# Performance work log

Hardware: AMD Instinct MI355X
Metric: run time of the kernel (lower is better)

The kernel has to match this reference:

```python
import jax, jax.numpy as jnp
import numpy as np

B, S, D, I, L, H, F = 4, 512, 768, 64, 2, 12, 3072
DH = D // H
LN_EPS = 1e-12


def setup_inputs() -> dict:
    key = jax.random.key(0)
    ks = jax.random.split(key, 24)
    nrm = lambda k, sh, s=0.02: jax.random.normal(k, sh, jnp.float32) * s
    return {
        'hs0': nrm(ks[0], (B, S, D), 1.0),
        'hs1': nrm(ks[1], (B, S, D), 1.0),
        'hs2': nrm(ks[2], (B, S, D), 1.0),
        'Wq': nrm(ks[3], (L, D, D)), 'bq': jnp.zeros((L, D), jnp.float32),
        'Wk': nrm(ks[4], (L, D, D)), 'bk': jnp.zeros((L, D), jnp.float32),
        'Wv': nrm(ks[5], (L, D, D)), 'bv': jnp.zeros((L, D), jnp.float32),
        'Wo': nrm(ks[6], (L, D, D)), 'bo': jnp.zeros((L, D), jnp.float32),
        'ln1_g': jnp.ones((L, D), jnp.float32), 'ln1_b': jnp.zeros((L, D), jnp.float32),
        'W1': nrm(ks[7], (L, D, F)), 'b1': jnp.zeros((L, F), jnp.float32),
        'W2': nrm(ks[8], (L, F, D)), 'b2': jnp.zeros((L, D), jnp.float32),
        'ln2_g': jnp.ones((L, D), jnp.float32), 'ln2_b': jnp.zeros((L, D), jnp.float32),
        'zero_context': nrm(ks[9], (D,), 1.0),
        'ck2tok_mask': jax.random.uniform(ks[10], (B, I, S)) > 0.7,  # True = token excluded from span
        'span_size_ids': jax.random.randint(ks[11], (B, I), 0, 10),
    }


def _ln(x, g, b):
    m = jnp.mean(x, axis=-1, keepdims=True)
    v = jnp.mean((x - m) ** 2, axis=-1, keepdims=True)
    return (x - m) * jax.lax.rsqrt(v + LN_EPS) * g + b


def _forward(hs0, hs1, Wq, bq, Wk, bk, Wv, bv, Wo, bo, ln1_g, ln1_b,
             W1, b1, W2, b2, ln2_g, ln2_b, zero_context, mask):
    # mask: [B,I,S] bool, True = excluded token
    zero_indic = jnp.all(mask, axis=-1)                 # [B,I] spans with no valid token
    mask = mask & ~zero_indic[:, :, None]               # unmask degenerate rows (replaced at end)
    # masked max pooling (init aggregation) -- [B,I,S,D] intermediate, traffic-bound
    pooled = jnp.max(jnp.where(mask[..., None], -jnp.inf, hs0[:, None, :, :]), axis=2)  # [B,I,D]
    ext = (mask.astype(jnp.float32) * -10000.0)[:, None, :, :]  # [B,1,I,S] extended attn mask
    q = pooled
    hs_list = (hs0, hs1)
    inv_sqrt_dh = np.float32(1.0 / np.sqrt(DH))
    for i in range(L):
        hs = hs_list[i]
        qh = (q @ Wq[i] + bq[i]).reshape(B, I, H, DH).transpose(0, 2, 1, 3)   # [B,H,I,DH]
        kh = (hs @ Wk[i] + bk[i]).reshape(B, S, H, DH).transpose(0, 2, 1, 3)  # [B,H,S,DH]
        vh = (hs @ Wv[i] + bv[i]).reshape(B, S, H, DH).transpose(0, 2, 1, 3)
        scores = jnp.einsum('bhid,bhsd->bhis', qh, kh) * inv_sqrt_dh + ext
        attn = jax.nn.softmax(scores, axis=-1)
        ctx = jnp.einsum('bhis,bhsd->bhid', attn, vh).transpose(0, 2, 1, 3).reshape(B, I, D)
        q = _ln(q + ctx @ Wo[i] + bo[i], ln1_g[i], ln1_b[i])
        ffn = jax.nn.gelu(q @ W1[i] + b1[i], approximate=False) @ W2[i] + b2[i]
        q = _ln(q + ffn, ln2_g[i], ln2_b[i])
    # zero-context substitution for empty spans
    return jnp.where(zero_indic[..., None], zero_context, q)


def reference(hs0, hs1, hs2, Wq, bq, Wk, bk, Wv, bv, Wo, bo, ln1_g, ln1_b,
              W1, b1, W2, b2, ln2_g, ln2_b, zero_context, ck2tok_mask, span_size_ids):
    # hs2 is the last entry of the (num_layers+1) slice; query layers 0..L-1 attend hs0..hs1.
    # span_size_ids unused since use_init_size_emb=False.
    del hs2, span_size_ids
    return _forward(hs0, hs1, Wq, bq, Wk, bk, Wv, bv, Wo, bo, ln1_g, ln1_b,
                    W1, b1, W2, b2, ln2_g, ln2_b, zero_context, ck2tok_mask)
```

## Files before the change

kernel.cpp:

```cpp
#include <hip/hip_runtime.h>
#include <hip/hip_bf16.h>
#include <math.h>

#define BB 4
#define SS 512
#define DD 768
#define II 64
#define LL 2
#define HH 12
#define FF 3072

using short8 = __attribute__((ext_vector_type(8))) short;
using f32x4  = __attribute__((ext_vector_type(4))) float;

__device__ __forceinline__ unsigned short f2bf(float x) {
  return __builtin_bit_cast(unsigned short, __float2bfloat16(x));
}

__device__ __forceinline__ void gload_lds16(const void* g, void* l) {
  __builtin_amdgcn_global_load_lds((const __attribute__((address_space(1))) unsigned int*)g,
                                   (__attribute__((address_space(3))) unsigned int*)l, 16, 0, 0);
}

__global__ __launch_bounds__(256) void castmask_kernel(
    const float* __restrict__ hs0, const float* __restrict__ hs1,
    unsigned short* __restrict__ hsb0, unsigned short* __restrict__ hsb1,
    const int* __restrict__ mask, int* __restrict__ zi,
    unsigned long long* __restrict__ pmask, unsigned char* __restrict__ emask) {
  int id = blockIdx.x, t = threadIdx.x;
  if (id < 1536) {
    int idx = id * 256 + t;
    float4 va = ((const float4*)hs0)[idx];
    float4 vb = ((const float4*)hs1)[idx];
    union { unsigned short u[4]; uint2 v; } pa, pb;
    pa.u[0] = f2bf(va.x); pa.u[1] = f2bf(va.y); pa.u[2] = f2bf(va.z); pa.u[3] = f2bf(va.w);
    pb.u[0] = f2bf(vb.x); pb.u[1] = f2bf(vb.y); pb.u[2] = f2bf(vb.z); pb.u[3] = f2bf(vb.w);
    ((uint2*)hsb0)[idx] = pa.v;
    ((uint2*)hsb1)[idx] = pb.v;
  } else {
    int bi = id - 1536;
    int w = t >> 6;
    const int* mrow = mask + (size_t)bi * SS;
    int m0v = mrow[t], m1v = mrow[t + 256];
    int incl = (m0v == 0) | (m1v == 0);
    int any = __syncthreads_or(incl);
    int z = !any;
    unsigned long long w0 = __ballot(z || (m0v == 0));
    unsigned long long w1 = __ballot(z || (m1v == 0));
    if ((t & 63) == 0) {
      pmask[bi * 8 + w] = w0;
      pmask[bi * 8 + 4 + w] = w1;
      if (t == 0) zi[bi] = z;
    }
    emask[(size_t)bi * SS + t] = (unsigned char)((!z) & (m0v != 0));
    emask[(size_t)bi * SS + t + 256] = (unsigned char)((!z) & (m1v != 0));
  }
}

struct TC { const float* s[6]; };

__global__ __launch_bounds__(256) void tcast_kernel(TC src, unsigned short* __restrict__ WT4,
                                                    unsigned short* __restrict__ W1T,
                                                    unsigned short* __restrict__ W2T) {
  __shared__ float smem[8192];
  int id = blockIdx.x, t = threadIdx.x;
  const float* Ws; unsigned short* WTs; int K, N, k0, n0;
  if (id < 576) {
    int z = id / 72, rem = id - z * 72;
    int widx = z >> 1, l = z & 1;
    Ws = src.s[widx] + (size_t)l * DD * DD;
    WTs = WT4 + ((size_t)widx * 2 + l) * DD * DD;
    K = DD; N = DD; k0 = (rem / 6) * 64; n0 = (rem % 6) * 128;
  } else if (id < 1152) {
    int j = id - 576, l = j / 288, rem = j - l * 288;
    Ws = src.s[4] + (size_t)l * DD * FF;
    WTs = W1T + (size_t)l * FF * DD;
    K = DD; N = FF; k0 = (rem / 24) * 64; n0 = (rem % 24) * 128;
  } else {
    int j = id - 1152, l = j / 288, rem = j - l * 288;
    Ws = src.s[5] + (size_t)l * FF * DD;
    WTs = W2T + (size_t)l * DD * FF;
    K = FF; N = DD; k0 = (rem / 6) * 64; n0 = (rem % 6) * 128;
  }
  int w = t >> 6, lane = t & 63;
  #pragma unroll
  for (int cc = 0; cc < 8; ++cc) {
    int c = w * 8 + cc;
    int row = c * 2 + (lane >> 5);
    int cbyte = (lane & 31) * 16;
    int scb = cbyte ^ ((row & 7) << 4);
    gload_lds16((const char*)(Ws + (size_t)(k0 + row) * N + n0) + scb, (char*)smem + c * 1024);
  }
  __syncthreads();
  int n = t >> 1, kh = t & 1;
  union { unsigned short u[32]; uint4 v4[4]; } pk;
  #pragma unroll
  for (int i = 0; i < 32; ++i) {
    int kl = kh * 32 + i;
    float f = *(const float*)((const char*)smem + kl * 512 + ((n * 4) ^ ((kl & 7) << 4)));
    pk.u[i] = f2bf(f);
  }
  uint4* dst = (uint4*)(WTs + (size_t)(n0 + n) * K + k0 + kh * 32);
  dst[0] = pk.v4[0]; dst[1] = pk.v4[1]; dst[2] = pk.v4[2]; dst[3] = pk.v4[3];
}

__global__ __launch_bounds__(256) void pool3_kernel(const float* __restrict__ hs0,
                                                    const unsigned char* __restrict__ emask,
                                                    float* __restrict__ qf,
                                                    unsigned short* __restrict__ qb) {
  __shared__ float eadd[SS];
  int bi = blockIdx.x, dz = blockIdx.y;
  int b = bi >> 6, t = threadIdx.x;
  if (t < 128) {
    uchar4 e4 = ((const uchar4*)(emask + (size_t)bi * SS))[t];
    const float NEG = -__builtin_inff();
    eadd[t * 4 + 0] = e4.x ? NEG : 0.0f;
    eadd[t * 4 + 1] = e4.y ? NEG : 0.0f;
    eadd[t * 4 + 2] = e4.z ? NEG : 0.0f;
    eadd[t * 4 + 3] = e4.w ? NEG : 0.0f;
  }
  __syncthreads();
  const float* hb = hs0 + (size_t)b * SS * DD + dz * 256 + t;
  float m[8];
  #pragma unroll
  for (int j = 0; j < 8; ++j) m[j] = -3.4e38f;
  for (int s0 = 0; s0 < SS; s0 += 8) {
    #pragma unroll
    for (int j = 0; j < 8; ++j)
      m[j] = fmaxf(m[j], hb[(size_t)(s0 + j) * DD] + eadd[s0 + j]);
  }
  float mm = fmaxf(fmaxf(fmaxf(m[0], m[1]), fmaxf(m[2], m[3])),
                   fmaxf(fmaxf(m[4], m[5]), fmaxf(m[6], m[7])));
  size_t o = (size_t)bi * DD + dz * 256 + t;
  qf[o] = mm;
  qb[o] = f2bf(mm);
}

struct GB { const unsigned short* A; const unsigned short* Bt; const float* bias; void* C;
            int M; int N; int rowbias; };

template <int GELU, int OUTBF>
__global__ __launch_bounds__(256) void gemm_nt(GB g0, GB g1, GB g2, GB g3, int K) {
  __shared__ unsigned short Al[2][128 * 64];
  __shared__ unsigned short Bl[2][128 * 64];
  GB g = (blockIdx.z == 0) ? g0 : (blockIdx.z == 1) ? g1 : (blockIdx.z == 2) ? g2 : g3;
  int bm = blockIdx.x, bn = blockIdx.y;
  if (blockIdx.z & 1) { bm = blockIdx.y; bn = blockIdx.x; }
  if (bm * 128 >= g.M) return;
  int t = threadIdx.x, w = t >> 6, lane = t & 63;
  int hi = lane >> 4, lo = lane & 15;
  int wr = w >> 1, wc = w & 1;
  f32x4 acc[4][4] = {};
  const char* Abase = (const char*)g.A + (size_t)(bm * 128) * (size_t)K * 2;
  const char* Bbase = (const char*)g.Bt + (size_t)(bn * 128) * (size_t)K * 2;
  int rowbytes = K * 2;
  int KT = K >> 6;
  auto STAGE = [&](int buf, int kt) {
    int k0b = kt * 128;
    #pragma unroll
    for (int c = 0; c < 4; ++c) {
      int base = (c * 4 + w) << 10;
      int o = base + lane * 16;
      int row = o >> 7, cb = o & 127;
      int scb = cb ^ ((row & 7) << 4);
      gload_lds16(Abase + (size_t)row * rowbytes + (k0b + scb), (char*)Al[buf] + base);
      gload_lds16(Bbase + (size_t)row * rowbytes + (k0b + scb), (char*)Bl[buf] + base);
    }
  };
  STAGE(0, 0);
  asm volatile("s_waitcnt vmcnt(0)" ::: "memory");
  __builtin_amdgcn_s_barrier();
  int cur = 0;
  for (int kt = 0; kt < KT; ++kt) {
    if (kt + 1 < KT) STAGE(cur ^ 1, kt + 1);
    #pragma unroll
    for (int kk = 0; kk < 2; ++kk) {
      short8 av[4], bv_[4];
      #pragma unroll
      for (int mi = 0; mi < 4; ++mi) {
        int r = wr * 64 + mi * 16 + lo;
        av[mi] = *(const short8*)((const char*)Al[cur] + r * 128 + ((kk * 64 + hi * 16) ^ ((r & 7) << 4)));
      }
      #pragma unroll
      for (int ni = 0; ni < 4; ++ni) {
        int r = wc * 64 + ni * 16 + lo;
        bv_[ni] = *(const short8*)((const char*)Bl[cur] + r * 128 + ((kk * 64 + hi * 16) ^ ((r & 7) << 4)));
      }
      #pragma unroll
      for (int mi = 0; mi < 4; ++mi)
        #pragma unroll
        for (int ni = 0; ni < 4; ++ni)
          acc[mi][ni] = __builtin_amdgcn_mfma_f32_16x16x32_bf16(av[mi], bv_[ni], acc[mi][ni], 0, 0, 0);
    }
    if (kt + 1 < KT) {
      asm volatile("s_waitcnt vmcnt(0)" ::: "memory");
      __builtin_amdgcn_s_barrier();
      cur ^= 1;
    }
  }
  int mbase = bm * 128 + wr * 64;
  int nbase = bn * 128 + wc * 64;
  #pragma unroll
  for (int mi = 0; mi < 4; ++mi)
    #pragma unroll
    for (int ni = 0; ni < 4; ++ni)
      #pragma unroll
      for (int r = 0; r < 4; ++r) {
        int gm = mbase + mi * 16 + hi * 4 + r;
        int gn = nbase + ni * 16 + lo;
        float v = acc[mi][ni][r] + (g.rowbias ? g.bias[gm] : g.bias[gn]);
        if (GELU) v = 0.5f * v * (1.0f + erff(v * 0.70710678118654752f));
        if (OUTBF) ((unsigned short*)g.C)[(size_t)gm * g.N + gn] = f2bf(v);
        else       ((float*)g.C)[(size_t)gm * g.N + gn] = v;
      }
}

template <int GELU, int OUTBF, int PARTIAL>
__global__ __launch_bounds__(256) void gemm_sk(GB g, int K, int kLen) {
  __shared__ unsigned short Al[2][64 * 64];
  __shared__ unsigned short Bl[2][64 * 64];
  int bm = blockIdx.x, bn = blockIdx.y, bz = blockIdx.z;
  int t = threadIdx.x, w = t >> 6, lane = t & 63;
  int hi = lane >> 4, lo = lane & 15;
  int wr = w >> 1, wc = w & 1;
  f32x4 acc[2][2] = {};
  size_t rb = (size_t)K * 2;
  const char* Abase = (const char*)g.A + (size_t)(bm * 64) * rb + (size_t)bz * kLen * 2;
  const char* Bbase = (const char*)g.Bt + (size_t)(bn * 64) * rb + (size_t)bz * kLen * 2;
  int KT = kLen >> 6;
  auto STAGE = [&](int buf, int kt) {
    int k0b = kt * 128;
    #pragma unroll
    for (int c = 0; c < 2; ++c) {
      int base = (c * 4 + w) << 10;
      int o = base + lane * 16;
      int row = o >> 7, cb = o & 127;
      int scb = cb ^ ((row & 7) << 4);
      gload_lds16(Abase + (size_t)row * rb + (k0b + scb), (char*)Al[buf] + base);
      gload_lds16(Bbase + (size_t)row * rb + (k0b + scb), (char*)Bl[buf] + base);
    }
  };
  STAGE(0, 0);
  asm volatile("s_waitcnt vmcnt(0)" ::: "memory");
  __builtin_amdgcn_s_barrier();
  int cur = 0;
  for (int kt = 0; kt < KT; ++kt) {
    if (kt + 1 < KT) STAGE(cur ^ 1, kt + 1);
    #pragma unroll
    for (int kk = 0; kk < 2; ++kk) {
      short8 av[2], bv_[2];
      #pragma unroll
      for (int mi = 0; mi < 2; ++mi) {
        int r = wr * 32 + mi * 16 + lo;
        av[mi] = *(const short8*)((const char*)Al[cur] + r * 128 + ((kk * 64 + hi * 16) ^ ((r & 7) << 4)));
      }
      #pragma unroll
      for (int ni = 0; ni < 2; ++ni) {
        int r = wc * 32 + ni * 16 + lo;
        bv_[ni] = *(const short8*)((const char*)Bl[cur] + r * 128 + ((kk * 64 + hi * 16) ^ ((r & 7) << 4)));
      }
      #pragma unroll
      for (int mi = 0; mi < 2; ++mi)
        #pragma unroll
        for (int ni = 0; ni < 2; ++ni)
          acc[mi][ni] = __builtin_amdgcn_mfma_f32_16x16x32_bf16(av[mi], bv_[ni], acc[mi][ni], 0, 0, 0);
    }
    if (kt + 1 < KT) {
      asm volatile("s_waitcnt vmcnt(0)" ::: "memory");
      __builtin_amdgcn_s_barrier();
      cur ^= 1;
    }
  }
  int mbase = bm * 64 + wr * 32;
  int nbase = bn * 64 + wc * 32;
  #pragma unroll
  for (int mi = 0; mi < 2; ++mi)
    #pragma unroll
    for (int ni = 0; ni < 2; ++ni)
      #pragma unroll
      for (int r = 0; r < 4; ++r) {
        int gm = mbase + mi * 16 + hi * 4 + r;
        int gn = nbase + ni * 16 + lo;
        if (PARTIAL) {
          ((float*)g.C)[((size_t)bz * g.M + gm) * g.N + gn] = acc[mi][ni][r];
        } else {
          float v = acc[mi][ni][r] + g.bias[gn];
          if (GELU) v = 0.5f * v * (1.0f + erff(v * 0.70710678118654752f));
          if (OUTBF) ((unsigned short*)g.C)[(size_t)gm * g.N + gn] = f2bf(v);
          else       ((float*)g.C)[(size_t)gm * g.N + gn] = v;
        }
      }
}

#define ATTN_LDS 145664
__global__ __launch_bounds__(256) void attn_kernel(
    const unsigned short* __restrict__ qbuf, const unsigned short* __restrict__ WqTl,
    const float* __restrict__ bql, const unsigned short* __restrict__ khb,
    const unsigned short* __restrict__ vTall, const unsigned long long* __restrict__ pmask,
    unsigned short* __restrict__ ctx) {
  extern __shared__ char lds[];
  char* Qd = lds;
  char* KP = lds + 8192;
  char* Vd = lds + 8192 + 65536;
  unsigned long long* pm = (unsigned long long*)(lds + 139264);
  float* red  = (float*)(lds + 143360);
  float* red2 = (float*)(lds + 144384);
  float* rnv  = (float*)(lds + 145408);
  int bh = blockIdx.x;
  int b = bh / HH, h = bh - b * HH;
  int t = threadIdx.x, w = t >> 6, l = t & 63, hi = l >> 4, lo = l & 15;
  int o16 = l * 16, ro = o16 >> 7, cb = o16 & 127;

  const char* vsrc = (const char*)vTall + (size_t)(h * 64) * 4096 + (size_t)b * 1024;
  #pragma unroll
  for (int rr = 0; rr < 16; ++rr) {
    int rv = w * 16 + rr;
    gload_lds16(vsrc + (size_t)rv * 4096 + ((l * 16) ^ ((rv & 7) << 4)), Vd + rv * 1024);
  }
  if (w == 0) {
    const char* psrc = (const char*)pmask + (size_t)b * 4096;
    #pragma unroll
    for (int c = 0; c < 4; ++c) gload_lds16(psrc + c * 1024 + l * 16, (char*)pm + c * 1024);
  }

  const char* Aq = (const char*)qbuf + (size_t)(b * II) * 1536;
  const char* Bq = (const char*)WqTl + (size_t)(h * 64) * 1536;
  f32x4 qacc[4] = {};
  #pragma unroll
  for (int cc = 0; cc < 2; ++cc) {
    int ch = w * 2 + cc, row = ch * 8 + ro;
    int scb = cb ^ ((row & 7) << 4);
    gload_lds16(Aq + (size_t)row * 1536 + scb, KP + ch * 1024);
    gload_lds16(Bq + (size_t)row * 1536 + scb, KP + 8192 + ch * 1024);
  }
  __syncthreads();
  for (int kt = 0; kt < 12; ++kt) {
    int cur = (kt & 1) * 16384;
    if (kt < 11) {
      int nxt = ((kt + 1) & 1) * 16384;
      int kb = (kt + 1) * 128;
      #pragma unroll
      for (int cc = 0; cc < 2; ++cc) {
        int ch = w * 2 + cc, row = ch * 8 + ro;
        int scb = kb + (cb ^ ((row & 7) << 4));
        gload_lds16(Aq + (size_t)row * 1536 + scb, KP + nxt + ch * 1024);
        gload_lds16(Bq + (size_t)row * 1536 + scb, KP + nxt + 8192 + ch * 1024);
      }
    }
    #pragma unroll
    for (int kk = 0; kk < 2; ++kk) {
      int ra = w * 16 + lo;
      short8 av = *(const short8*)(KP + cur + ra * 128 + ((kk * 64 + hi * 16) ^ ((ra & 7) << 4)));
      #pragma unroll
      for (int ni = 0; ni < 4; ++ni) {
        int rb2 = ni * 16 + lo;
        short8 bv = *(const short8*)(KP + cur + 8192 + rb2 * 128 + ((kk * 64 + hi * 16) ^ ((rb2 & 7) << 4)));
        qacc[ni] = __builtin_amdgcn_mfma_f32_16x16x32_bf16(av, bv, qacc[ni], 0, 0, 0);
      }
    }
    __syncthreads();
  }
  #pragma unroll
  for (int ni = 0; ni < 4; ++ni)
    #pragma unroll
    for (int r = 0; r < 4; ++r) {
      int row = w * 16 + hi * 4 + r, col = ni * 16 + lo;
      float v = qacc[ni][r] + bql[h * 64 + col];
      *(unsigned short*)(Qd + row * 128 + ((col * 2) ^ ((row & 7) << 4))) = f2bf(v);
    }
  const char* Ks = (const char*)khb + (size_t)(b * SS) * 1536 + h * 128;
  #pragma unroll
  for (int cc = 0; cc < 16; ++cc) {
    int ch = w * 16 + cc, row = ch * 8 + ro;
    int scb = cb ^ ((row & 7) << 4);
    gload_lds16(Ks + (size_t)row * 1536 + scb, KP + ch * 1024);
  }
  __syncthreads();

  f32x4 acc[4][8] = {};
  #pragma unroll
  for (int kk = 0; kk < 2; ++kk) {
    short8 av[4];
    #pragma unroll
    for (int mi = 0; mi < 4; ++mi) {
      int ra = mi * 16 + lo;
      av[mi] = *(const short8*)(Qd + ra * 128 + ((kk * 64 + hi * 16) ^ ((ra & 7) << 4)));
    }
    #pragma unroll
    for (int ni = 0; ni < 8; ++ni) {
      int rk = w * 128 + ni * 16 + lo;
      short8 bv = *(const short8*)(KP + rk * 128 + ((kk * 64 + hi * 16) ^ ((rk & 7) << 4)));
      #pragma unroll
      for (int mi = 0; mi < 4; ++mi)
        acc[mi][ni] = __builtin_amdgcn_mfma_f32_16x16x32_bf16(av[mi], bv, acc[mi][ni], 0, 0, 0);
    }
  }
  #pragma unroll
  for (int mi = 0; mi < 4; ++mi)
    #pragma unroll
    for (int r = 0; r < 4; ++r) {
      float m = acc[mi][0][r];
      #pragma unroll
      for (int ni = 1; ni < 8; ++ni) m = fmaxf(m, acc[mi][ni][r]);
      #pragma unroll
      for (int xm = 1; xm <= 8; xm <<= 1) m = fmaxf(m, __shfl_xor(m, xm));
      if (lo == 0) red[(mi * 16 + hi * 4 + r) * 4 + w] = m;
    }
  __syncthreads();
  #pragma unroll
  for (int mi = 0; mi < 4; ++mi)
    #pragma unroll
    for (int r = 0; r < 4; ++r) {
      int row = mi * 16 + hi * 4 + r;
      float4 rm4 = *(const float4*)&red[row * 4];
      float gm = fmaxf(fmaxf(rm4.x, rm4.y), fmaxf(rm4.z, rm4.w));
      unsigned long long w0 = pm[row * 8 + w * 2 + 0];
      unsigned long long w1 = pm[row * 8 + w * 2 + 1];
      float s = 0.f;
      #pragma unroll
      for (int ni = 0; ni < 8; ++ni) {
        int sl = ni * 16 + lo;
        unsigned long long word = (sl < 64) ? w0 : w1;
        float in = ((word >> (sl & 63)) & 1ull) ? 1.0f : 0.0f;
        float e = __expf((acc[mi][ni][r] - gm) * 0.125f) * in;
        s += e;
        int sbyte = w * 256 + ni * 32 + lo * 2;
        *(unsigned short*)(KP + row * 1024 + (sbyte ^ ((row & 7) << 4))) = f2bf(e);
      }
      #pragma unroll
      for (int xm = 1; xm <= 8; xm <<= 1) s += __shfl_xor(s, xm);
      if (lo == 0) red2[row * 4 + w] = s;
    }
  __syncthreads();
  if (w == 0 && lo == 0) {
    #pragma unroll
    for (int mi = 0; mi < 4; ++mi)
      #pragma unroll
      for (int r = 0; r < 4; ++r) {
        int row = mi * 16 + hi * 4 + r;
        float4 s4 = *(const float4*)&red2[row * 4];
        rnv[row] = 1.0f / ((s4.x + s4.y) + (s4.z + s4.w));
      }
  }
  __syncthreads();
  f32x4 pacc[4] = {};
  for (int kk = 0; kk < 16; ++kk) {
    int rv = w * 16 + lo;
    short8 bv = *(const short8*)(Vd + rv * 1024 + ((kk * 64 + hi * 16) ^ ((rv & 7) << 4)));
    #pragma unroll
    for (int mi = 0; mi < 4; ++mi) {
      int ra = mi * 16 + lo;
      short8 av = *(const short8*)(KP + ra * 1024 + ((kk * 64 + hi * 16) ^ ((ra & 7) << 4)));
      pacc[mi] = __builtin_amdgcn_mfma_f32_16x16x32_bf16(av, bv, pacc[mi], 0, 0, 0);
    }
  }
  #pragma unroll
  for (int mi = 0; mi < 4; ++mi)
    #pragma unroll
    for (int r = 0; r < 4; ++r) {
      int row = mi * 16 + hi * 4 + r;
      ctx[(size_t)(b * II + row) * DD + h * 64 + w * 16 + lo] = f2bf(pacc[mi][r] * rnv[row]);
    }
}

template <int FINAL, int NP>
__global__ __launch_bounds__(256) void ln_kernel(const float* __restrict__ x, const float* __restrict__ y,
                                                 const float* __restrict__ gb,
                                                 const float* __restrict__ g, const float* __restrict__ bb,
                                                 float* __restrict__ qf, unsigned short* __restrict__ qb,
                                                 const int* __restrict__ zi, const float* __restrict__ zc,
                                                 float* __restrict__ out) {
  __shared__ float r1[4], r2[4];
  const int MN = BB * II * DD;
  int r = blockIdx.x, t = threadIdx.x;
  size_t o = (size_t)r * DD;
  float v0 = x[o + t] + gb[t];
  float v1 = x[o + t + 256] + gb[t + 256];
  float v2 = x[o + t + 512] + gb[t + 512];
  #pragma unroll
  for (int p = 0; p < NP; ++p) {
    size_t po = (size_t)p * MN + o;
    v0 += y[po + t];
    v1 += y[po + t + 256];
    v2 += y[po + t + 512];
  }
  float s = v0 + v1 + v2, ss = v0 * v0 + v1 * v1 + v2 * v2;
  #pragma unroll
  for (int o2 = 32; o2; o2 >>= 1) { s += __shfl_xor(s, o2); ss += __shfl_xor(ss, o2); }
  if ((t & 63) == 0) { r1[t >> 6] = s; r2[t >> 6] = ss; }
  __syncthreads();
  s = r1[0] + r1[1] + r1[2] + r1[3];
  ss = r2[0] + r2[1] + r2[2] + r2[3];
  float mean = s * (1.0f / DD);
  float var = ss * (1.0f / DD) - mean * mean;
  float inv = rsqrtf(var + 1e-12f);
  float w0 = (v0 - mean) * inv * g[t] + bb[t];
  float w1 = (v1 - mean) * inv * g[t + 256] + bb[t + 256];
  float w2 = (v2 - mean) * inv * g[t + 512] + bb[t + 512];
  if (FINAL) {
    int z = zi[r];
    out[o + t] = z ? zc[t] : w0;
    out[o + t + 256] = z ? zc[t + 256] : w1;
    out[o + t + 512] = z ? zc[t + 512] : w2;
  } else {
    qf[o + t] = w0; qf[o + t + 256] = w1; qf[o + t + 512] = w2;
    qb[o + t] = f2bf(w0); qb[o + t + 256] = f2bf(w1); qb[o + t + 512] = f2bf(w2);
  }
}

extern "C" void kernel_launch(void* const* d_in, const int* in_sizes, int n_in,
                              void* d_out, int out_size, void* d_ws, size_t ws_size,
                              hipStream_t stream) {
  (void)in_sizes; (void)n_in; (void)out_size; (void)ws_size;
  const float* hs0 = (const float*)d_in[0];
  const float* hs1 = (const float*)d_in[1];
  const float* Wq  = (const float*)d_in[3];
  const float* bq  = (const float*)d_in[4];
  const float* Wk  = (const float*)d_in[5];
  const float* bk  = (const float*)d_in[6];
  const float* Wv  = (const float*)d_in[7];
  const float* bv  = (const float*)d_in[8];
  const float* Wo  = (const float*)d_in[9];
  const float* bo  = (const float*)d_in[10];
  const float* ln1g = (const float*)d_in[11];
  const float* ln1b = (const float*)d_in[12];
  const float* W1  = (const float*)d_in[13];
  const float* b1  = (const float*)d_in[14];
  const float* W2  = (const float*)d_in[15];
  const float* b2  = (const float*)d_in[16];
  const float* ln2g = (const float*)d_in[17];
  const float* ln2b = (const float*)d_in[18];
  const float* zc  = (const float*)d_in[19];
  const int*   mask = (const int*)d_in[20];

  char* ws = (char*)d_ws;
  size_t off = 0;
  auto alloc = [&](size_t bytes) { size_t o = off; off += (bytes + 255) & ~(size_t)255; return o; };

  unsigned short* WT4 = (unsigned short*)(ws + alloc((size_t)4 * LL * DD * DD * 2));
  unsigned short* W1T = (unsigned short*)(ws + alloc((size_t)LL * FF * DD * 2));
  unsigned short* W2T = (unsigned short*)(ws + alloc((size_t)LL * DD * FF * 2));
  unsigned short* hsb = (unsigned short*)(ws + alloc((size_t)2 * BB * SS * DD * 2));
  float*          qf  = (float*)(ws + alloc((size_t)BB * II * DD * 4));
  unsigned short* qb  = (unsigned short*)(ws + alloc((size_t)BB * II * DD * 2));
  unsigned short* khb = (unsigned short*)(ws + alloc((size_t)LL * BB * SS * DD * 2));
  unsigned short* vTall = (unsigned short*)(ws + alloc((size_t)LL * DD * BB * SS * 2));
  unsigned short* ctxb = (unsigned short*)(ws + alloc((size_t)BB * II * DD * 2));
  float*          att_o = (float*)(ws + alloc((size_t)2 * BB * II * DD * 4));
  unsigned short* ffh = (unsigned short*)(ws + alloc((size_t)BB * II * FF * 2));
  float*          ffo = (float*)(ws + alloc((size_t)4 * BB * II * DD * 4));
  unsigned long long* pmask = (unsigned long long*)(ws + alloc((size_t)BB * II * 8 * 8));
  unsigned char*  emask = (unsigned char*)(ws + alloc((size_t)BB * II * SS));
  int*            zib = (int*)(ws + alloc((size_t)BB * II * 4));

  unsigned short* WqT = WT4 + 0 * (size_t)LL * DD * DD;
  unsigned short* WkT = WT4 + 1 * (size_t)LL * DD * DD;
  unsigned short* WvT = WT4 + 2 * (size_t)LL * DD * DD;
  unsigned short* WoT = WT4 + 3 * (size_t)LL * DD * DD;

  (void)hipFuncSetAttribute((const void*)attn_kernel,
                            hipFuncAttributeMaxDynamicSharedMemorySize, ATTN_LDS);

  castmask_kernel<<<1536 + 256, 256, 0, stream>>>(hs0, hs1, hsb, hsb + (size_t)BB * SS * DD,
                                                  mask, zib, pmask, emask);
  TC tc = { { Wq, Wk, Wv, Wo, W1, W2 } };
  tcast_kernel<<<1728, 256, 0, stream>>>(tc, WT4, W1T, W2T);
  pool3_kernel<<<dim3(BB * II, 3), 256, 0, stream>>>(hs0, emask, qf, qb);

  {
    const unsigned short* h0 = hsb;
    const unsigned short* h1 = hsb + (size_t)BB * SS * DD;
    GB gK0 = { h0, WkT, bk, khb, BB * SS, DD, 0 };
    GB gV0 = { WvT, h0, bv, vTall, DD, BB * SS, 1 };
    GB gK1 = { h1, WkT + (size_t)DD * DD, bk + DD, khb + (size_t)BB * SS * DD, BB * SS, DD, 0 };
    GB gV1 = { WvT + (size_t)DD * DD, h1, bv + DD, vTall + (size_t)DD * BB * SS, DD, BB * SS, 1 };
    gemm_nt<0, 1><<<dim3(16, 6, 4), 256, 0, stream>>>(gK0, gV0, gK1, gV1, DD);
  }

  for (int l = 0; l < LL; ++l) {
    const unsigned short* khl = khb + (size_t)l * BB * SS * DD;
    const unsigned short* vTl = vTall + (size_t)l * DD * BB * SS;
    attn_kernel<<<dim3(BB * HH), 256, ATTN_LDS, stream>>>(
        qb, WqT + (size_t)l * DD * DD, bq + l * DD, khl, vTl, pmask, ctxb);
    GB gO = { ctxb, WoT + (size_t)l * DD * DD, nullptr, att_o, BB * II, DD, 0 };
    gemm_sk<0, 0, 1><<<dim3(4, 12, 2), 256, 0, stream>>>(gO, DD, DD / 2);
    ln_kernel<0, 2><<<BB * II, 256, 0, stream>>>(qf, att_o, bo + l * DD,
                                                 ln1g + l * DD, ln1b + l * DD, qf, qb,
                                                 nullptr, nullptr, nullptr);
    GB gF1 = { qb, W1T + (size_t)l * FF * DD, b1 + l * FF, ffh, BB * II, FF, 0 };
    gemm_sk<1, 1, 0><<<dim3(4, FF / 64, 1), 256, 0, stream>>>(gF1, DD, DD);
    GB gF2 = { ffh, W2T + (size_t)l * DD * FF, nullptr, ffo, BB * II, DD, 0 };
    gemm_sk<0, 0, 1><<<dim3(4, 12, 4), 256, 0, stream>>>(gF2, FF, FF / 4);
    if (l == 0)
      ln_kernel<0, 4><<<BB * II, 256, 0, stream>>>(qf, ffo, b2 + l * DD,
                                                   ln2g + l * DD, ln2b + l * DD, qf, qb,
                                                   nullptr, nullptr, nullptr);
    else
      ln_kernel<1, 4><<<BB * II, 256, 0, stream>>>(qf, ffo, b2 + l * DD,
                                                   ln2g + l * DD, ln2b + l * DD, nullptr, nullptr,
                                                   zib, zc, (float*)d_out);
  }
}
```

Baseline: 183.1 us.

## Fuse post-attention GEMMs and layernorms into persistent kernel with grid barriers

Replaces the per-layer sequence of five launches (Wo GEMM, LN1, FFN1 GEMM, FFN2 GEMM, LN2) with one persistent kernel of 192 blocks that separates the stages with atomic-counter grid barriers. It also merges the weight transpose-cast and the activation cast/mask kernels into a single prep launch. The aim is to cut kernel launch overhead and tail gaps on a small-M problem. In exchange, it relies on all 192 blocks being co-resident for the spin barriers, adds a memset for the counters, and leaves barrier spin costs between stages.

```diff
diff --git a/kernel.cpp b/kernel.cpp
--- a/kernel.cpp
+++ b/kernel.cpp
@@ -9,6 +9,7 @@
 #define LL 2
 #define HH 12
 #define FF 3072
+#define MEGA_NB 192
 
 using short8 = __attribute__((ext_vector_type(8))) short;
 using f32x4  = __attribute__((ext_vector_type(4))) float;
@@ -22,14 +23,72 @@
                                    (__attribute__((address_space(3))) unsigned int*)l, 16, 0, 0);
 }
 
-__global__ __launch_bounds__(256) void castmask_kernel(
+__device__ __forceinline__ void gbar(unsigned* cnt, unsigned nb) {
+  __syncthreads();
+  if (threadIdx.x == 0) {
+    __threadfence();
+    __hip_atomic_fetch_add(cnt, 1u, __ATOMIC_RELAXED, __HIP_MEMORY_SCOPE_AGENT);
+    while (__hip_atomic_load(cnt, __ATOMIC_RELAXED, __HIP_MEMORY_SCOPE_AGENT) < nb)
+      __builtin_amdgcn_s_sleep(2);
+    __threadfence();
+  }
+  __syncthreads();
+}
+
+struct TC { const float* s[6]; };
+struct GB { const unsigned short* A; const unsigned short* Bt; const float* bias; void* C;
+            int M; int N; int rowbias; };
+
+__global__ __launch_bounds__(256) void prep1_kernel(
+    TC src, unsigned short* __restrict__ WT4, unsigned short* __restrict__ W1T,
+    unsigned short* __restrict__ W2T,
     const float* __restrict__ hs0, const float* __restrict__ hs1,
     unsigned short* __restrict__ hsb0, unsigned short* __restrict__ hsb1,
     const int* __restrict__ mask, int* __restrict__ zi,
     unsigned long long* __restrict__ pmask, unsigned char* __restrict__ emask) {
+  __shared__ float smem[8192];
   int id = blockIdx.x, t = threadIdx.x;
-  if (id < 1536) {
-    int idx = id * 256 + t;
+  if (id < 1728) {
+    const float* Ws; unsigned short* WTs; int K, N, k0, n0;
+    if (id < 576) {
+      int z = id / 72, rem = id - z * 72;
+      int widx = z >> 1, l = z & 1;
+      Ws = src.s[widx] + (size_t)l * DD * DD;
+      WTs = WT4 + ((size_t)widx * 2 + l) * DD * DD;
+      K = DD; N = DD; k0 = (rem / 6) * 64; n0 = (rem % 6) * 128;
+    } else if (id < 1152) {
+      int j = id - 576, l = j / 288, rem = j - l * 288;
+      Ws = src.s[4] + (size_t)l * DD * FF;
+      WTs = W1T + (size_t)l * FF * DD;
+      K = DD; N = FF; k0 = (rem / 24) * 64; n0 = (rem % 24) * 128;
+    } else {
+      int j = id - 1152, l = j / 288, rem = j - l * 288;
+      Ws = src.s[5] + (size_t)l * FF * DD;
+      WTs = W2T + (size_t)l * DD * FF;
+      K = FF; N = DD; k0 = (rem / 6) * 64; n0 = (rem % 6) * 128;
+    }
+    int w = t >> 6, lane = t & 63;
+    #pragma unroll
+    for (int cc = 0; cc < 8; ++cc) {
+      int c = w * 8 + cc;
+      int row = c * 2 + (lane >> 5);
+      int cbyte = (lane & 31) * 16;
+      int scb = cbyte ^ ((row & 7) << 4);
+      gload_lds16((const char*)(Ws + (size_t)(k0 + row) * N + n0) + scb, (char*)smem + c * 1024);
+    }
+    __syncthreads();
+    int n = t >> 1, kh = t & 1;
+    union { unsigned short u[32]; uint4 v4[4]; } pk;
+    #pragma unroll
+    for (int i = 0; i < 32; ++i) {
+      int kl = kh * 32 + i;
+      float f = *(const float*)((const char*)smem + kl * 512 + ((n * 4) ^ ((kl & 7) << 4)));
+      pk.u[i] = f2bf(f);
+    }
+    uint4* dst = (uint4*)(WTs + (size_t)(n0 + n) * K + k0 + kh * 32);
+    dst[0] = pk.v4[0]; dst[1] = pk.v4[1]; dst[2] = pk.v4[2]; dst[3] = pk.v4[3];
+  } else if (id < 3264) {
+    int idx = (id - 1728) * 256 + t;
     float4 va = ((const float4*)hs0)[idx];
     float4 vb = ((const float4*)hs1)[idx];
     union { unsigned short u[4]; uint2 v; } pa, pb;
@@ -38,7 +97,7 @@
     ((uint2*)hsb0)[idx] = pa.v;
     ((uint2*)hsb1)[idx] = pb.v;
   } else {
-    int bi = id - 1536;
+    int bi = id - 3264;
     int w = t >> 6;
     const int* mrow = mask + (size_t)bi * SS;
     int m0v = mrow[t], m1v = mrow[t + 256];
@@ -55,53 +114,6 @@
     emask[(size_t)bi * SS + t] = (unsigned char)((!z) & (m0v != 0));
     emask[(size_t)bi * SS + t + 256] = (unsigned char)((!z) & (m1v != 0));
   }
-}
-
-struct TC { const float* s[6]; };
-
-__global__ __launch_bounds__(256) void tcast_kernel(TC src, unsigned short* __restrict__ WT4,
-                                                    unsigned short* __restrict__ W1T,
-                                                    unsigned short* __restrict__ W2T) {
-  __shared__ float smem[8192];
-  int id = blockIdx.x, t = threadIdx.x;
-  const float* Ws; unsigned short* WTs; int K, N, k0, n0;
-  if (id < 576) {
-    int z = id / 72, rem = id - z * 72;
-    int widx = z >> 1, l = z & 1;
-    Ws = src.s[widx] + (size_t)l * DD * DD;
-    WTs = WT4 + ((size_t)widx * 2 + l) * DD * DD;
-    K = DD; N = DD; k0 = (rem / 6) * 64; n0 = (rem % 6) * 128;
-  } else if (id < 1152) {
-    int j = id - 576, l = j / 288, rem = j - l * 288;
-    Ws = src.s[4] + (size_t)l * DD * FF;
-    WTs = W1T + (size_t)l * FF * DD;
-    K = DD; N = FF; k0 = (rem / 24) * 64; n0 = (rem % 24) * 128;
-  } else {
-    int j = id - 1152, l = j / 288, rem = j - l * 288;
-    Ws = src.s[5] + (size_t)l * FF * DD;
-    WTs = W2T + (size_t)l * DD * FF;
-    K = FF; N = DD; k0 = (rem / 6) * 64; n0 = (rem % 6) * 128;
-  }
-  int w = t >> 6, lane = t & 63;
-  #pragma unroll
-  for (int cc = 0; cc < 8; ++cc) {
-    int c = w * 8 + cc;
-    int row = c * 2 + (lane >> 5);
-    int cbyte = (lane & 31) * 16;
-    int scb = cbyte ^ ((row & 7) << 4);
-    gload_lds16((const char*)(Ws + (size_t)(k0 + row) * N + n0) + scb, (char*)smem + c * 1024);
-  }
-  __syncthreads();
-  int n = t >> 1, kh = t & 1;
-  union { unsigned short u[32]; uint4 v4[4]; } pk;
-  #pragma unroll
-  for (int i = 0; i < 32; ++i) {
-    int kl = kh * 32 + i;
-    float f = *(const float*)((const char*)smem + kl * 512 + ((n * 4) ^ ((kl & 7) << 4)));
-    pk.u[i] = f2bf(f);
-  }
-  uint4* dst = (uint4*)(WTs + (size_t)(n0 + n) * K + k0 + kh * 32);
-  dst[0] = pk.v4[0]; dst[1] = pk.v4[1]; dst[2] = pk.v4[2]; dst[3] = pk.v4[3];
 }
 
 __global__ __launch_bounds__(256) void pool3_kernel(const float* __restrict__ hs0,
@@ -135,9 +147,6 @@
   qf[o] = mm;
   qb[o] = f2bf(mm);
 }
-
-struct GB { const unsigned short* A; const unsigned short* Bt; const float* bias; void* C;
-            int M; int N; int rowbias; };
 
 template <int GELU, int OUTBF>
 __global__ __launch_bounds__(256) void gemm_nt(GB g0, GB g1, GB g2, GB g3, int K) {
@@ -216,10 +225,10 @@
 }
 
 template <int GELU, int OUTBF, int PARTIAL>
-__global__ __launch_bounds__(256) void gemm_sk(GB g, int K, int kLen) {
-  __shared__ unsigned short Al[2][64 * 64];
-  __shared__ unsigned short Bl[2][64 * 64];
-  int bm = blockIdx.x, bn = blockIdx.y, bz = blockIdx.z;
+__device__ __forceinline__ void gemm64_body(char* shm, GB g, int K, int kLen,
+                                            int bm, int bn, int bz) {
+  char* Al = shm;
+  char* Bl = shm + 16384;
   int t = threadIdx.x, w = t >> 6, lane = t & 63;
   int hi = lane >> 4, lo = lane & 15;
   int wr = w >> 1, wc = w & 1;
@@ -236,8 +245,8 @@
       int o = base + lane * 16;
       int row = o >> 7, cb = o & 127;
       int scb = cb ^ ((row & 7) << 4);
-      gload_lds16(Abase + (size_t)row * rb + (k0b + scb), (char*)Al[buf] + base);
-      gload_lds16(Bbase + (size_t)row * rb + (k0b + scb), (char*)Bl[buf] + base);
+      gload_lds16(Abase + (size_t)row * rb + (k0b + scb), Al + buf * 8192 + base);
+      gload_lds16(Bbase + (size_t)row * rb + (k0b + scb), Bl + buf * 8192 + base);
     }
   };
   STAGE(0, 0);
@@ -252,12 +261,12 @@
       #pragma unroll
       for (int mi = 0; mi < 2; ++mi) {
         int r = wr * 32 + mi * 16 + lo;
-        av[mi] = *(const short8*)((const char*)Al[cur] + r * 128 + ((kk * 64 + hi * 16) ^ ((r & 7) << 4)));
+        av[mi] = *(const short8*)(Al + cur * 8192 + r * 128 + ((kk * 64 + hi * 16) ^ ((r & 7) << 4)));
       }
       #pragma unroll
       for (int ni = 0; ni < 2; ++ni) {
         int r = wc * 32 + ni * 16 + lo;
-        bv_[ni] = *(const short8*)((const char*)Bl[cur] + r * 128 + ((kk * 64 + hi * 16) ^ ((r & 7) << 4)));
+        bv_[ni] = *(const short8*)(Bl + cur * 8192 + r * 128 + ((kk * 64 + hi * 16) ^ ((r & 7) << 4)));
       }
       #pragma unroll
       for (int mi = 0; mi < 2; ++mi)
@@ -290,6 +299,92 @@
           else       ((float*)g.C)[(size_t)gm * g.N + gn] = v;
         }
       }
+}
+
+template <int FINAL, int NP>
+__device__ __forceinline__ void ln_body(int r, const float* x, const float* y, const float* gb,
+                                        const float* g, const float* bb,
+                                        float* qf, unsigned short* qb,
+                                        const int* zi, const float* zc, float* out,
+                                        float* r1, float* r2) {
+  const int MN = BB * II * DD;
+  int t = threadIdx.x;
+  size_t o = (size_t)r * DD;
+  float v0 = x[o + t] + gb[t];
+  float v1 = x[o + t + 256] + gb[t + 256];
+  float v2 = x[o + t + 512] + gb[t + 512];
+  #pragma unroll
+  for (int p = 0; p < NP; ++p) {
+    size_t po = (size_t)p * MN + o;
+    v0 += y[po + t];
+    v1 += y[po + t + 256];
+    v2 += y[po + t + 512];
+  }
+  float s = v0 + v1 + v2, ss = v0 * v0 + v1 * v1 + v2 * v2;
+  #pragma unroll
+  for (int o2 = 32; o2; o2 >>= 1) { s += __shfl_xor(s, o2); ss += __shfl_xor(ss, o2); }
+  if ((t & 63) == 0) { r1[t >> 6] = s; r2[t >> 6] = ss; }
+  __syncthreads();
+  s = r1[0] + r1[1] + r1[2] + r1[3];
+  ss = r2[0] + r2[1] + r2[2] + r2[3];
+  float mean = s * (1.0f / DD);
+  float var = ss * (1.0f / DD) - mean * mean;
+  float inv = rsqrtf(var + 1e-12f);
+  float w0 = (v0 - mean) * inv * g[t] + bb[t];
+  float w1 = (v1 - mean) * inv * g[t + 256] + bb[t + 256];
+  float w2 = (v2 - mean) * inv * g[t + 512] + bb[t + 512];
+  if (FINAL) {
+    int z = zi[r];
+    out[o + t] = z ? zc[t] : w0;
+    out[o + t + 256] = z ? zc[t + 256] : w1;
+    out[o + t + 512] = z ? zc[t + 512] : w2;
+  } else {
+    qf[o + t] = w0; qf[o + t + 256] = w1; qf[o + t + 512] = w2;
+    qb[o + t] = f2bf(w0); qb[o + t + 256] = f2bf(w1); qb[o + t + 512] = f2bf(w2);
+  }
+  __syncthreads();
+}
+
+struct MegaArgs {
+  unsigned* cnt;
+  const unsigned short* ctx; const unsigned short* WoT; const float* bo;
+  float* att_o; float* qf; unsigned short* qb;
+  const float* ln1g; const float* ln1b;
+  const unsigned short* W1T; const float* b1; unsigned short* ffh;
+  const unsigned short* W2T; const float* b2; float* ffo;
+  const float* ln2g; const float* ln2b;
+  int fin; const int* zi; const float* zc; float* out;
+};
+
+__global__ __launch_bounds__(256) void mega_kernel(MegaArgs a) {
+  __shared__ char shm[32768];
+  __shared__ float r1[4], r2[4];
+  int bid = blockIdx.x;
+  if (bid < 96) {
+    GB gO = { a.ctx, a.WoT, nullptr, a.att_o, BB * II, DD, 0 };
+    gemm64_body<0, 0, 1>(shm, gO, DD, DD / 2, bid & 3, (bid >> 2) % 12, bid / 48);
+  }
+  gbar(a.cnt + 0, MEGA_NB);
+  for (int r = bid; r < BB * II; r += MEGA_NB)
+    ln_body<0, 2>(r, a.qf, a.att_o, a.bo, a.ln1g, a.ln1b, a.qf, a.qb, nullptr, nullptr, nullptr, r1, r2);
+  gbar(a.cnt + 1, MEGA_NB);
+  {
+    GB gF1 = { a.qb, a.W1T, a.b1, a.ffh, BB * II, FF, 0 };
+    gemm64_body<1, 1, 0>(shm, gF1, DD, DD, bid & 3, bid >> 2, 0);
+  }
+  gbar(a.cnt + 2, MEGA_NB);
+  {
+    GB gF2 = { a.ffh, a.W2T, nullptr, a.ffo, BB * II, DD, 0 };
+    gemm64_body<0, 0, 1>(shm, gF2, FF, FF / 4, bid & 3, (bid >> 2) % 12, bid / 48);
+  }
+  gbar(a.cnt + 3, MEGA_NB);
+  if (a.fin) {
+    for (int r = bid; r < BB * II; r += MEGA_NB)
+      ln_body<1, 4>(r, a.qf, a.ffo, a.b2, a.ln2g, a.ln2b, nullptr, nullptr, a.zi, a.zc, a.out, r1, r2);
+  } else {
+    for (int r = bid; r < BB * II; r += MEGA_NB)
+      ln_body<0, 4>(r, a.qf, a.ffo, a.b2, a.ln2g, a.ln2b, a.qf, a.qb, nullptr, nullptr, nullptr, r1, r2);
+  }
 }
 
 #define ATTN_LDS 145664
@@ -461,51 +556,6 @@
       int row = mi * 16 + hi * 4 + r;
       ctx[(size_t)(b * II + row) * DD + h * 64 + w * 16 + lo] = f2bf(pacc[mi][r] * rnv[row]);
     }
-}
-
-template <int FINAL, int NP>
-__global__ __launch_bounds__(256) void ln_kernel(const float* __restrict__ x, const float* __restrict__ y,
-                                                 const float* __restrict__ gb,
-                                                 const float* __restrict__ g, const float* __restrict__ bb,
-                                                 float* __restrict__ qf, unsigned short* __restrict__ qb,
-                                                 const int* __restrict__ zi, const float* __restrict__ zc,
-                                                 float* __restrict__ out) {
-  __shared__ float r1[4], r2[4];
-  const int MN = BB * II * DD;
-  int r = blockIdx.x, t = threadIdx.x;
-  size_t o = (size_t)r * DD;
-  float v0 = x[o + t] + gb[t];
-  float v1 = x[o + t + 256] + gb[t + 256];
-  float v2 = x[o + t + 512] + gb[t + 512];
-  #pragma unroll
-  for (int p = 0; p < NP; ++p) {
-    size_t po = (size_t)p * MN + o;
-    v0 += y[po + t];
-    v1 += y[po + t + 256];
-    v2 += y[po + t + 512];
-  }
-  float s = v0 + v1 + v2, ss = v0 * v0 + v1 * v1 + v2 * v2;
-  #pragma unroll
-  for (int o2 = 32; o2; o2 >>= 1) { s += __shfl_xor(s, o2); ss += __shfl_xor(ss, o2); }
-  if ((t & 63) == 0) { r1[t >> 6] = s; r2[t >> 6] = ss; }
-  __syncthreads();
-  s = r1[0] + r1[1] + r1[2] + r1[3];
-  ss = r2[0] + r2[1] + r2[2] + r2[3];
-  float mean = s * (1.0f / DD);
-  float var = ss * (1.0f / DD) - mean * mean;
-  float inv = rsqrtf(var + 1e-12f);
-  float w0 = (v0 - mean) * inv * g[t] + bb[t];
-  float w1 = (v1 - mean) * inv * g[t + 256] + bb[t + 256];
-  float w2 = (v2 - mean) * inv * g[t + 512] + bb[t + 512];
-  if (FINAL) {
-    int z = zi[r];
-    out[o + t] = z ? zc[t] : w0;
-    out[o + t + 256] = z ? zc[t + 256] : w1;
-    out[o + t + 512] = z ? zc[t + 512] : w2;
-  } else {
-    qf[o + t] = w0; qf[o + t + 256] = w1; qf[o + t + 512] = w2;
-    qb[o + t] = f2bf(w0); qb[o + t + 256] = f2bf(w1); qb[o + t + 512] = f2bf(w2);
-  }
 }
 
 extern "C" void kernel_launch(void* const* d_in, const int* in_sizes, int n_in,
@@ -552,6 +602,7 @@
   unsigned long long* pmask = (unsigned long long*)(ws + alloc((size_t)BB * II * 8 * 8));
   unsigned char*  emask = (unsigned char*)(ws + alloc((size_t)BB * II * SS));
   int*            zib = (int*)(ws + alloc((size_t)BB * II * 4));
+  unsigned*       cnts = (unsigned*)(ws + alloc(8 * sizeof(unsigned)));
 
   unsigned short* WqT = WT4 + 0 * (size_t)LL * DD * DD;
   unsigned short* WkT = WT4 + 1 * (size_t)LL * DD * DD;
@@ -561,10 +612,12 @@
   (void)hipFuncSetAttribute((const void*)attn_kernel,
                             hipFuncAttributeMaxDynamicSharedMemorySize, ATTN_LDS);
 
-  castmask_kernel<<<1536 + 256, 256, 0, stream>>>(hs0, hs1, hsb, hsb + (size_t)BB * SS * DD,
-                                                  mask, zib, pmask, emask);
+  hipMemsetAsync(cnts, 0, 8 * sizeof(unsigned), stream);
+
   TC tc = { { Wq, Wk, Wv, Wo, W1, W2 } };
-  tcast_kernel<<<1728, 256, 0, stream>>>(tc, WT4, W1T, W2T);
+  prep1_kernel<<<3520, 256, 0, stream>>>(tc, WT4, W1T, W2T, hs0, hs1,
+                                         hsb, hsb + (size_t)BB * SS * DD,
+                                         mask, zib, pmask, emask);
   pool3_kernel<<<dim3(BB * II, 3), 256, 0, stream>>>(hs0, emask, qf, qb);
 
   {
@@ -582,22 +635,15 @@
     const unsigned short* vTl = vTall + (size_t)l * DD * BB * SS;
     attn_kernel<<<dim3(BB * HH), 256, ATTN_LDS, stream>>>(
         qb, WqT + (size_t)l * DD * DD, bq + l * DD, khl, vTl, pmask, ctxb);
-    GB gO = { ctxb, WoT + (size_t)l * DD * DD, nullptr, att_o, BB * II, DD, 0 };
-    gemm_sk<0, 0, 1><<<dim3(4, 12, 2), 256, 0, stream>>>(gO, DD, DD / 2);
-    ln_kernel<0, 2><<<BB * II, 256, 0, stream>>>(qf, att_o, bo + l * DD,
-                                                 ln1g + l * DD, ln1b + l * DD, qf, qb,
-                                                 nullptr, nullptr, nullptr);
-    GB gF1 = { qb, W1T + (size_t)l * FF * DD, b1 + l * FF, ffh, BB * II, FF, 0 };
-    gemm_sk<1, 1, 0><<<dim3(4, FF / 64, 1), 256, 0, stream>>>(gF1, DD, DD);
-    GB gF2 = { ffh, W2T + (size_t)l * DD * FF, nullptr, ffo, BB * II, DD, 0 };
-    gemm_sk<0, 0, 1><<<dim3(4, 12, 4), 256, 0, stream>>>(gF2, FF, FF / 4);
-    if (l == 0)
-      ln_kernel<0, 4><<<BB * II, 256, 0, stream>>>(qf, ffo, b2 + l * DD,
-                                                   ln2g + l * DD, ln2b + l * DD, qf, qb,
-                                                   nullptr, nullptr, nullptr);
-    else
-      ln_kernel<1, 4><<<BB * II, 256, 0, stream>>>(qf, ffo, b2 + l * DD,
-                                                   ln2g + l * DD, ln2b + l * DD, nullptr, nullptr,
-                                                   zib, zc, (float*)d_out);
-  }
-}
+    MegaArgs ma;
+    ma.cnt = cnts + l * 4;
+    ma.ctx = ctxb; ma.WoT = WoT + (size_t)l * DD * DD; ma.bo = bo + l * DD;
+    ma.att_o = att_o; ma.qf = qf; ma.qb = qb;
+    ma.ln1g = ln1g + l * DD; ma.ln1b = ln1b + l * DD;
+    ma.W1T = W1T + (size_t)l * FF * DD; ma.b1 = b1 + l * FF; ma.ffh = ffh;
+    ma.W2T = W2T + (size_t)l * DD * FF; ma.b2 = b2 + l * DD; ma.ffo = ffo;
+    ma.ln2g = ln2g + l * DD; ma.ln2b = ln2b + l * DD;
+    ma.fin = (l == LL - 1); ma.zi = zib; ma.zc = zc; ma.out = (float*)d_out;
+    mega_kernel<<<MEGA_NB, 256, 0, stream>>>(ma);
+  }
+}
```

Result: slower. 291.1 us (+58.9%).
